# Performance work log

Measured on AMD Instinct MI355X. Metric: run time of the kernel, lower is better.

## Reference

```python
import jax, jax.numpy as jnp
import numpy as np

NEG_INF = -1e9  # matches the torch module's masked_fill value of -1000000000.0


def setup_inputs() -> dict:
    key = jax.random.key(0)
    kq, kk, kv, km = jax.random.split(key, 4)
    b, h, L, d = 2, 16, 2048, 64
    q = jax.random.normal(kq, (b, h, L, d), dtype=jnp.float32)
    k = jax.random.normal(kk, (b, h, L, d), dtype=jnp.float32)
    v = jax.random.normal(kv, (b, h, L, d), dtype=jnp.float32)
    attn_mask = jax.random.randint(km, (b, 1, L, L), 0, 2, dtype=jnp.int32)
    return {"q": q, "k": k, "v": v, "attn_mask": attn_mask}


def reference(q, k, v, attn_mask):
    # att = q @ k^T / sqrt(d)   -> [b, h, Lq, Lk]
    scale = 1.0 / jnp.sqrt(jnp.asarray(q.shape[-1], q.dtype))
    att = jnp.einsum("bhqd,bhkd->bhqk", q, k) * scale
    # masked positions (mask == 0) filled with -1e9 before softmax
    att = jnp.where(attn_mask == 0, jnp.asarray(NEG_INF, att.dtype), att)
    att = jax.nn.softmax(att, axis=-1)
    # x = att @ v -> [b, h, Lq, d]
    return jnp.einsum("bhqk,bhkd->bhqd", att, v)
```

## Files before the change

kernel.cpp:

```cpp
#include <hip/hip_runtime.h>


typedef unsigned int u32;
typedef unsigned short u16;
typedef unsigned long long u64;

#define BH 32
#define Lseq 2048
#define Dh 64

#define KSCALE 0.125f
#define BIASF  -12.0f
#define NEGF   -1.0e9f

typedef __attribute__((ext_vector_type(8))) short frag_ab;
typedef __attribute__((ext_vector_type(16))) float f32x16;

__device__ __forceinline__ u16 f2bf(float f) {
    u32 u = __float_as_uint(f);
    u32 r = u + 0x7FFFu + ((u >> 16) & 1u);
    return (u16)(r >> 16);
}

__device__ __forceinline__ u32 pk2bf(float a, float b) {
    return (u32)f2bf(a) | ((u32)f2bf(b) << 16);
}

__device__ __forceinline__ u32 cvtpk_bf16(float lo, float hi) {
    u32 r;
    asm("v_cvt_pk_bf16_f32 %0, %1, %2" : "=v"(r) : "v"(lo), "v"(hi));
    return r;
}

__device__ __forceinline__ void pl32swap(u32 &a, u32 &b) {
#if __has_builtin(__builtin_amdgcn_permlane32_swap)
    typedef __attribute__((ext_vector_type(2))) unsigned int uvec2;
    uvec2 r = __builtin_amdgcn_permlane32_swap(a, b, false, false);
    a = r[0]; b = r[1];
#else
    asm("v_permlane32_swap_b32 %0, %1" : "+v"(a), "+v"(b));
#endif
}

__device__ __forceinline__ frag_ab mkfrag(u32 a, u32 b, u32 c, u32 d) {
    union { u32 w[4]; frag_ab f; } u;
    u.w[0] = a; u.w[1] = b; u.w[2] = c; u.w[3] = d;
    return u.f;
}

__global__ __launch_bounds__(256) void prep(
    const float* __restrict__ k, const float* __restrict__ v,
    const int* __restrict__ mask,
    u16* __restrict__ kfm, u16* __restrict__ vfm, u64* __restrict__ bm)
{
    const int blk = blockIdx.x, tid = threadIdx.x;
    if (blk < 1024) {
        const int bh = blk >> 5, kt = blk & 31;
        #pragma unroll
        for (int i = 0; i < 2; i++) {
            int cid = tid + 256 * i;
            int half = cid >> 8, ko = (cid >> 6) & 3, lane = cid & 63;
            int key = kt * 64 + half * 32 + (lane & 31);
            int d0 = ko * 16 + 8 * (lane >> 5);
            const float* src = k + ((size_t)(bh * Lseq + key)) * Dh + d0;
            float4 f0 = *(const float4*)src;
            float4 f1 = *(const float4*)(src + 4);
            uint4 o;
            o.x = pk2bf(f0.x * KSCALE, f0.y * KSCALE);
            o.y = pk2bf(f0.z * KSCALE, f0.w * KSCALE);
            o.z = pk2bf(f1.x * KSCALE, f1.y * KSCALE);
            o.w = pk2bf(f1.z * KSCALE, f1.w * KSCALE);
            *(uint4*)(kfm + ((size_t)(blk * 8 + half * 4 + ko) * 64 + lane) * 8) = o;
        }
    } else if (blk < 2048) {
        __shared__ u16 T[64 * 72];
        int job = blk - 1024;
        int bh = job >> 5, kt = job & 31;
        #pragma unroll
        for (int i = 0; i < 4; i++) {
            int idx = tid + 256 * i;
            int key = idx >> 4, ds = idx & 15;
            float4 f = *(const float4*)(v + ((size_t)(bh * Lseq + kt * 64 + key)) * Dh + ds * 4);
            int d0 = ds * 4;
            T[(d0 + 0) * 72 + key] = f2bf(f.x);
            T[(d0 + 1) * 72 + key] = f2bf(f.y);
            T[(d0 + 2) * 72 + key] = f2bf(f.z);
            T[(d0 + 3) * 72 + key] = f2bf(f.w);
        }
        __syncthreads();
        #pragma unroll
        for (int i = 0; i < 2; i++) {
            int cid = tid + 256 * i;
            int dhalf = cid >> 8, ks = (cid >> 6) & 3, lane = cid & 63;
            int d = dhalf * 32 + (lane & 31);
            int koff = ks * 16 + 8 * (lane >> 5);
            uint4 c = *(const uint4*)&T[d * 72 + koff];
            *(uint4*)(vfm + ((size_t)(job * 8 + dhalf * 4 + ks) * 64 + lane) * 8) = c;
        }
    } else {
        int wv = (blk - 2048) * 4 + (tid >> 6);
        int lane = tid & 63;
        #pragma unroll
        for (int i = 0; i < 16; i++) {
            int widx = wv * 16 + i;
            int rowp = widx >> 5, kt = widx & 31;
            int val = mask[(size_t)rowp * Lseq + kt * 64 + lane];
            u64 bal = __ballot(val != 0);
            if (lane == 0) bm[(size_t)kt * 4096 + rowp] = bal;
        }
    }
}

__global__ __launch_bounds__(512, 2)
void attn_mfma(const float* __restrict__ qg, const u16* __restrict__ kfm,
               const u16* __restrict__ vfm, const u64* __restrict__ bm,
               float* __restrict__ outg)
{
    const int bid = blockIdx.x;
    const int swz = (bid & 7) * 64 + (bid >> 3);
    const int bh = swz >> 4, b = bh >> 4;
    const int q0 = (swz & 15) * 128;
    const int tid = threadIdx.x;
    const int wave = tid >> 6, lane = tid & 63;
    const int g = wave & 3;
    const int h = wave >> 2;
    const int kt0 = h * 16;
    const int ql = lane & 31, hi = lane >> 5;
    const int sh4 = hi * 4;

    __shared__ float mrg[4][64][34];

    const u16* kbase = kfm + ((size_t)bh << 17) + lane * 8;
    const u16* vbase = vfm + ((size_t)bh << 17) + lane * 8;
    const int mrow = b * 2048 + q0 + 32 * g + ql;

    frag_ab qf[4];
    #pragma unroll
    for (int ko = 0; ko < 4; ko++) {
        const float* p = qg + ((size_t)bh * Lseq + q0 + 32 * g + ql) * Dh + ko * 16 + 8 * hi;
        float4 f0 = *(const float4*)p;
        float4 f1 = *(const float4*)(p + 4);
        union { u32 w[4]; frag_ab f; } uq;
        uq.w[0] = pk2bf(f0.x, f0.y);
        uq.w[1] = pk2bf(f0.z, f0.w);
        uq.w[2] = pk2bf(f1.x, f1.y);
        uq.w[3] = pk2bf(f1.z, f1.w);
        qf[ko] = uq.f;
    }

    f32x16 o0, o1;
    #pragma unroll
    for (int i = 0; i < 16; i++) { o0[i] = 0.f; o1[i] = 0.f; }
    float l_run = 0.f;

    u64 mw = bm[(size_t)kt0 * 4096 + mrow];

    #pragma unroll 1
    for (int kti = 0; kti < 16; ++kti) {
        const int kt = kt0 + kti;
        frag_ab kf[8];
        #pragma unroll
        for (int j = 0; j < 8; j++)
            kf[j] = *(const frag_ab*)(kbase + (size_t)(kt * 8 + j) * 512);
        const int ktn = (kti < 15) ? (kt + 1) : kt;
        u64 mw_nx = bm[(size_t)ktn * 4096 + mrow];

        u64 shm = mw >> sh4;
        u32 w0 = (u32)shm, w1 = (u32)(shm >> 32);
        f32x16 s0, s1;
        #pragma unroll
        for (int r = 0; r < 16; r++) {
            const int bit = (r & 3) + 8 * (r >> 2);
            s0[r] = (w0 & (1u << bit)) ? BIASF : NEGF;
            s1[r] = (w1 & (1u << bit)) ? BIASF : NEGF;
        }
        __builtin_amdgcn_s_setprio(1);
        #pragma unroll
        for (int ko = 0; ko < 4; ko++) {
            s0 = __builtin_amdgcn_mfma_f32_32x32x16_bf16(kf[ko],     qf[ko], s0, 0, 0, 0);
            s1 = __builtin_amdgcn_mfma_f32_32x32x16_bf16(kf[4 + ko], qf[ko], s1, 0, 0, 0);
        }
        __builtin_amdgcn_s_setprio(0);
        frag_ab vf[8];
        #pragma unroll
        for (int j = 0; j < 8; j++)
            vf[j] = *(const frag_ab*)(vbase + (size_t)(kt * 8 + j) * 512);

        u32 y0[8], y1[8];
        #pragma unroll
        for (int j = 0; j < 8; j++) {
            float pa = __expf(s0[2 * j]);
            float pb = __expf(s0[2 * j + 1]);
            float pc = __expf(s1[2 * j]);
            float pd = __expf(s1[2 * j + 1]);
            l_run += (pa + pb) + (pc + pd);
            y0[j] = cvtpk_bf16(pa, pb);
            y1[j] = cvtpk_bf16(pc, pd);
        }
        pl32swap(y0[0], y0[2]); pl32swap(y0[1], y0[3]);
        pl32swap(y0[4], y0[6]); pl32swap(y0[5], y0[7]);
        pl32swap(y1[0], y1[2]); pl32swap(y1[1], y1[3]);
        pl32swap(y1[4], y1[6]); pl32swap(y1[5], y1[7]);
        frag_ab pf[4];
        pf[0] = mkfrag(y0[0], y0[1], y0[2], y0[3]);
        pf[1] = mkfrag(y0[4], y0[5], y0[6], y0[7]);
        pf[2] = mkfrag(y1[0], y1[1], y1[2], y1[3]);
        pf[3] = mkfrag(y1[4], y1[5], y1[6], y1[7]);

        __builtin_amdgcn_s_setprio(1);
        #pragma unroll
        for (int ks = 0; ks < 4; ks++) {
            o0 = __builtin_amdgcn_mfma_f32_32x32x16_bf16(vf[ks],     pf[ks], o0, 0, 0, 0);
            o1 = __builtin_amdgcn_mfma_f32_32x32x16_bf16(vf[4 + ks], pf[ks], o1, 0, 0, 0);
        }
        __builtin_amdgcn_s_setprio(0);
        mw = mw_nx;
    }

    if (h == 1) {
        #pragma unroll
        for (int i = 0; i < 16; i++) {
            mrg[g][lane][i] = o0[i];
            mrg[g][lane][16 + i] = o1[i];
        }
        mrg[g][lane][32] = l_run;
    }
    __syncthreads();
    if (h == 0) {
        #pragma unroll
        for (int i = 0; i < 16; i++) {
            o0[i] += mrg[g][lane][i];
            o1[i] += mrg[g][lane][16 + i];
        }
        float l = l_run + mrg[g][lane][32];
        l += __shfl_xor(l, 32);
        const float inv = 1.0f / l;
        float* orow = outg + ((size_t)bh * Lseq + q0 + 32 * g + ql) * Dh;
        #pragma unroll
        for (int q4 = 0; q4 < 4; q4++) {
            *(float4*)(orow + 8 * q4 + 4 * hi) =
                make_float4(o0[4 * q4 + 0] * inv, o0[4 * q4 + 1] * inv,
                            o0[4 * q4 + 2] * inv, o0[4 * q4 + 3] * inv);
            *(float4*)(orow + 32 + 8 * q4 + 4 * hi) =
                make_float4(o1[4 * q4 + 0] * inv, o1[4 * q4 + 1] * inv,
                            o1[4 * q4 + 2] * inv, o1[4 * q4 + 3] * inv);
        }
    }
}

extern "C" void kernel_launch(void* const* d_in, const int* in_sizes, int n_in,
                              void* d_out, int out_size, void* d_ws, size_t ws_size,
                              hipStream_t stream) {
    const float* q    = (const float*)d_in[0];
    const float* k    = (const float*)d_in[1];
    const float* v    = (const float*)d_in[2];
    const int*   mask = (const int*)d_in[3];
    float* out = (float*)d_out;

    char* ws = (char*)d_ws;
    u16* kfm = (u16*)(ws);
    u16* vfm = (u16*)(ws + 8388608);
    u64* bmp = (u64*)(ws + 16777216);

    hipLaunchKernelGGL(prep, dim3(4096), dim3(256), 0, stream, k, v, mask, kfm, vfm, bmp);
    hipLaunchKernelGGL(attn_mfma, dim3(512), dim3(512), 0, stream,
                       q, kfm, vfm, bmp, out);
}
```

Measured before the change: 171.4 us.

## Stage K/V tiles through double-buffered LDS with async global-to-LDS loads

K and V fragments are no longer loaded straight into registers from global memory by each wave. All 512 threads now cooperatively copy the next tile pair into a double-buffered 64KB shared buffer with global_load_lds, while the current tile is consumed from LDS. A block-wide barrier is added every iteration, and the merge scratch reuses the same buffer. The launch bound is raised to 4 blocks per CU to trade registers for occupancy, but 64KB of LDS per block may limit residency and the barriers add sync cost.

```diff
diff --git a/kernel.cpp b/kernel.cpp
--- a/kernel.cpp
+++ b/kernel.cpp
@@ -40,6 +40,12 @@
 #else
     asm("v_permlane32_swap_b32 %0, %1" : "+v"(a), "+v"(b));
 #endif
+}
+
+__device__ __forceinline__ void gl16(const void* g, void* l) {
+    __builtin_amdgcn_global_load_lds(
+        (const __attribute__((address_space(1))) u32*)g,
+        (__attribute__((address_space(3))) u32*)l, 16, 0, 0);
 }
 
 __device__ __forceinline__ frag_ab mkfrag(u32 a, u32 b, u32 c, u32 d) {
@@ -111,7 +117,8 @@
     }
 }
 
-__global__ __launch_bounds__(512, 2)
+
+__global__ __launch_bounds__(512, 4)
 void attn_mfma(const float* __restrict__ qg, const u16* __restrict__ kfm,
                const u16* __restrict__ vfm, const u64* __restrict__ bm,
                float* __restrict__ outg)
@@ -128,11 +135,24 @@
     const int ql = lane & 31, hi = lane >> 5;
     const int sh4 = hi * 4;
 
-    __shared__ float mrg[4][64][34];
-
-    const u16* kbase = kfm + ((size_t)bh << 17) + lane * 8;
-    const u16* vbase = vfm + ((size_t)bh << 17) + lane * 8;
+    __shared__ u16 smem[32768];
+    char* smem_c = (char*)smem;
+
+    const u16* sK = kfm + ((size_t)bh << 17) + (tid >> 6) * 512 + (tid & 63) * 8;
+    const u16* sV = vfm + ((size_t)bh << 17) + (tid >> 6) * 512 + (tid & 63) * 8;
+    const int d0 = (tid >> 6) * 1024 + (tid & 63) * 16;
+
+#define STAGE(DB, I) do {                                                    \
+    gl16(sK + (I) * 4096,         smem_c + (DB) * 32768 + d0);               \
+    gl16(sV + (I) * 4096,         smem_c + (DB) * 32768 + 8192 + d0);        \
+    gl16(sK + 65536 + (I) * 4096, smem_c + (DB) * 32768 + 16384 + d0);       \
+    gl16(sV + 65536 + (I) * 4096, smem_c + (DB) * 32768 + 24576 + d0);       \
+} while (0)
+
+    STAGE(0, 0);
+
     const int mrow = b * 2048 + q0 + 32 * g + ql;
+    u64 mw = bm[(size_t)kt0 * 4096 + mrow];
 
     frag_ab qf[4];
     #pragma unroll
@@ -153,16 +173,15 @@
     for (int i = 0; i < 16; i++) { o0[i] = 0.f; o1[i] = 0.f; }
     float l_run = 0.f;
 
-    u64 mw = bm[(size_t)kt0 * 4096 + mrow];
-
+    const int lbase = h * 16384 + lane * 16;
+
+    __syncthreads();
+
+    int db = 0;
     #pragma unroll 1
-    for (int kti = 0; kti < 16; ++kti) {
-        const int kt = kt0 + kti;
-        frag_ab kf[8];
-        #pragma unroll
-        for (int j = 0; j < 8; j++)
-            kf[j] = *(const frag_ab*)(kbase + (size_t)(kt * 8 + j) * 512);
-        const int ktn = (kti < 15) ? (kt + 1) : kt;
+    for (int i = 0; i < 16; ++i) {
+        if (i < 15) STAGE(db ^ 1, i + 1);
+        const int ktn = (i < 15) ? (kt0 + i + 1) : (kt0 + i);
         u64 mw_nx = bm[(size_t)ktn * 4096 + mrow];
 
         u64 shm = mw >> sh4;
@@ -177,14 +196,12 @@
         __builtin_amdgcn_s_setprio(1);
         #pragma unroll
         for (int ko = 0; ko < 4; ko++) {
-            s0 = __builtin_amdgcn_mfma_f32_32x32x16_bf16(kf[ko],     qf[ko], s0, 0, 0, 0);
-            s1 = __builtin_amdgcn_mfma_f32_32x32x16_bf16(kf[4 + ko], qf[ko], s1, 0, 0, 0);
+            frag_ab kf0 = *(const frag_ab*)(smem_c + db * 32768 + lbase + ko * 1024);
+            frag_ab kf1 = *(const frag_ab*)(smem_c + db * 32768 + lbase + (4 + ko) * 1024);
+            s0 = __builtin_amdgcn_mfma_f32_32x32x16_bf16(kf0, qf[ko], s0, 0, 0, 0);
+            s1 = __builtin_amdgcn_mfma_f32_32x32x16_bf16(kf1, qf[ko], s1, 0, 0, 0);
         }
         __builtin_amdgcn_s_setprio(0);
-        frag_ab vf[8];
-        #pragma unroll
-        for (int j = 0; j < 8; j++)
-            vf[j] = *(const frag_ab*)(vbase + (size_t)(kt * 8 + j) * 512);
 
         u32 y0[8], y1[8];
         #pragma unroll
@@ -210,29 +227,37 @@
         __builtin_amdgcn_s_setprio(1);
         #pragma unroll
         for (int ks = 0; ks < 4; ks++) {
-            o0 = __builtin_amdgcn_mfma_f32_32x32x16_bf16(vf[ks],     pf[ks], o0, 0, 0, 0);
-            o1 = __builtin_amdgcn_mfma_f32_32x32x16_bf16(vf[4 + ks], pf[ks], o1, 0, 0, 0);
+            frag_ab va = *(const frag_ab*)(smem_c + db * 32768 + 8192 + lbase + ks * 1024);
+            frag_ab vb = *(const frag_ab*)(smem_c + db * 32768 + 8192 + lbase + (4 + ks) * 1024);
+            o0 = __builtin_amdgcn_mfma_f32_32x32x16_bf16(va, pf[ks], o0, 0, 0, 0);
+            o1 = __builtin_amdgcn_mfma_f32_32x32x16_bf16(vb, pf[ks], o1, 0, 0, 0);
         }
         __builtin_amdgcn_s_setprio(0);
+
+        __syncthreads();
+        db ^= 1;
         mw = mw_nx;
     }
 
+    float* mrgf = (float*)smem_c;
     if (h == 1) {
+        float* row = mrgf + (g * 64 + lane) * 34;
         #pragma unroll
         for (int i = 0; i < 16; i++) {
-            mrg[g][lane][i] = o0[i];
-            mrg[g][lane][16 + i] = o1[i];
-        }
-        mrg[g][lane][32] = l_run;
+            row[i] = o0[i];
+            row[16 + i] = o1[i];
+        }
+        row[32] = l_run;
     }
     __syncthreads();
     if (h == 0) {
+        const float* row = mrgf + (g * 64 + lane) * 34;
         #pragma unroll
         for (int i = 0; i < 16; i++) {
-            o0[i] += mrg[g][lane][i];
-            o1[i] += mrg[g][lane][16 + i];
-        }
-        float l = l_run + mrg[g][lane][32];
+            o0[i] += row[i];
+            o1[i] += row[16 + i];
+        }
+        float l = l_run + row[32];
         l += __shfl_xor(l, 32);
         const float inv = 1.0f / l;
         float* orow = outg + ((size_t)bh * Lseq + q0 + 32 * g + ql) * Dh;
```

Measured after the change: 168.2 us. Within noise of the previous version (-1.9%).
